# Kernel tuning notes

Hardware: AMD Instinct MI355X
Metric: run time of the kernel (lower is better)

## Reference

```python
import jax, jax.numpy as jnp
import numpy as np

B, L, D = 4, 512, 2880          # packed sequences, tokens per seq, hidden
N, K, H = 64, 8, 64             # query heads, kv heads, head dim
G = N // K                      # GQA group size
WINDOW = 128                    # sliding window (gpt-oss window layer)
SM_SCALE = 1.0 / H ** 0.5
THETA = 150000.0
INIT_CTX = 4096.0
SCALING = 32.0
NTK_ALPHA = 1.0
NTK_BETA = 32.0
NEG = -1e30


def _rope_tables(positions):
    # GPT-OSS YaRN NTK-by-parts rotary tables.
    d_half = H // 2
    freq = THETA ** (jnp.arange(0, H, 2, dtype=jnp.float32) / H)
    concentration = 0.1 * np.log(SCALING) + 1.0
    low = d_half * np.log(INIT_CTX / (NTK_BETA * 2 * np.pi)) / np.log(THETA)
    high = d_half * np.log(INIT_CTX / (NTK_ALPHA * 2 * np.pi)) / np.log(THETA)
    interp = 1.0 / (SCALING * freq)
    extrap = 1.0 / freq
    ramp = jnp.clip((jnp.arange(d_half, dtype=jnp.float32) - low) / (high - low), 0.0, 1.0)
    blend = 1.0 - ramp
    inv_freq = interp * (1.0 - blend) + extrap * blend
    ang = positions.astype(jnp.float32)[:, None] * inv_freq[None, :]  # [T, H/2]
    return jnp.cos(ang) * concentration, jnp.sin(ang) * concentration


def _apply_rope(x, cos, sin):
    # x: [T, heads, H]; half-split rotation as in gpt-oss.
    x1, x2 = x[..., : H // 2], x[..., H // 2:]
    c, s = cos[:, None, :], sin[:, None, :]
    return jnp.concatenate([x1 * c - x2 * s, x2 * c + x1 * s], axis=-1)


def setup_inputs() -> dict:
    key = jax.random.key(0)
    ks = jax.random.split(key, 10)
    T = B * L
    return {
        "x": jax.random.normal(ks[0], (T, D), jnp.float32),
        "wq": jax.random.normal(ks[1], (D, N, H), jnp.float32) * 0.02,
        "bq": jax.random.normal(ks[2], (N, H), jnp.float32) * 0.02,
        "wk": jax.random.normal(ks[3], (D, K, H), jnp.float32) * 0.02,
        "bk": jax.random.normal(ks[4], (K, H), jnp.float32) * 0.02,
        "wv": jax.random.normal(ks[5], (D, K, H), jnp.float32) * 0.02,
        "bv": jax.random.normal(ks[6], (K, H), jnp.float32) * 0.02,
        "wo": jax.random.normal(ks[7], (N, H, D), jnp.float32) * 0.02,
        "bo": jax.random.normal(ks[8], (D,), jnp.float32) * 0.02,
        "sinks": jax.random.normal(ks[9], (N,), jnp.float32),
        "positions": jnp.tile(jnp.arange(L, dtype=jnp.int32), B),  # per-seq positions
    }


def reference(x, wq, bq, wk, bk, wv, bv, wo, bo, sinks, positions):
    # fused QKV projections
    q = jnp.einsum('td,dnh->tnh', x, wq) + bq            # [T,N,H]
    k = jnp.einsum('td,dkh->tkh', x, wk) + bk            # [T,K,H]
    v = jnp.einsum('td,dkh->tkh', x, wv) + bv            # [T,K,H]
    cos, sin = _rope_tables(positions)
    q = _apply_rope(q, cos, sin)
    k = _apply_rope(k, cos, sin)
    # unpack ragged tokens into [B, L, ...] (equal-length packed sequences)
    qb = q.reshape(B, L, K, G, H)
    kb = k.reshape(B, L, K, H)
    vb = v.reshape(B, L, K, H)
    s = jnp.einsum('blkgh,bmkh->bkglm', qb, kb) * SM_SCALE  # [B,K,G,L,L]
    pos = jnp.arange(L)
    delta = pos[:, None] - pos[None, :]
    allowed = (delta >= 0) & (delta < WINDOW)               # causal + sliding window
    s = jnp.where(allowed, s, NEG)
    # attention sinks: extra per-head logit joining the softmax denominator only
    sink = sinks.reshape(K, G)[None, :, :, None]            # [1,K,G,1]
    m = jnp.maximum(jnp.max(s, axis=-1), sink)              # [B,K,G,L]
    p = jnp.exp(s - m[..., None])
    denom = jnp.exp(sink - m) + jnp.sum(p, axis=-1)         # [B,K,G,L]
    o = jnp.einsum('bkglm,bmkh->blkgh', p, vb)
    o = o / jnp.transpose(denom, (0, 3, 1, 2))[..., None]   # [B,L,K,G,H]
    attn = o.reshape(B * L, N, H)
    return jnp.einsum('tnh,nhd->td', attn, wo) + bo         # [T,D]
```

## Files before the change

### kernel.cpp

```cpp
#include <hip/hip_runtime.h>
#include <hip/hip_bf16.h>

#define TB 4
#define TL 512
#define TD 2880
#define TN 64
#define TKH 8
#define TH 64
#define TG 8
#define TWIN 128
#define TT (TB*TL)

typedef unsigned short u16;
typedef __attribute__((ext_vector_type(8))) short bf16x8;
typedef __attribute__((ext_vector_type(4))) float f32x4;

__device__ __forceinline__ u16 f2b(float f) {
  unsigned u = __float_as_uint(f);
  u += 0x7fffu + ((u >> 16) & 1u);
  return (u16)(u >> 16);
}
__device__ __forceinline__ float b2f(u16 u) {
  return __uint_as_float(((unsigned)u) << 16);
}

__device__ __forceinline__ void load_lds16(const u16* g, u16* l) {
  __builtin_amdgcn_global_load_lds(
      (const __attribute__((address_space(1))) unsigned int*)g,
      (__attribute__((address_space(3))) unsigned int*)l, 16, 0, 0);
}

template<int BN>
__global__ __launch_bounds__(256, 4) void gemm_sn(
    const u16* __restrict__ A, const u16* __restrict__ Bt,
    const float* __restrict__ bias, void* __restrict__ Cv,
    int Kd, int Nc, int ldc, int out_bf16, int nx)
{
  constexpr int NF = BN / 32;
  __shared__ u16 As[128*64];
  __shared__ u16 Bs[BN*64];

  const int tid  = threadIdx.x;
  const int lane = tid & 63;
  const int wave = tid >> 6;

  int id = blockIdx.x;
  const int cpx = gridDim.x >> 3;
  id = (id & 7)*cpx + (id >> 3);
  const int rgsz = nx << 3;
  const int rg   = id / rgsz;
  const int rem  = id - rg*rgsz;
  const int bm = (rg*8 + (rem & 7)) * 128;
  const int bn = (rem >> 3) * BN;

  const int wr = (wave >> 1) * 64;
  const int wc = (wave & 1) * (BN/2);

  f32x4 acc[4][NF];
#pragma unroll
  for (int i = 0; i < 4; ++i)
#pragma unroll
    for (int j = 0; j < NF; ++j) acc[i][j] = (f32x4){0.f,0.f,0.f,0.f};

  const int rr   = tid >> 3;
  const int sseg = (tid & 7) ^ (rr & 7);
  const u16* aS = A  + (size_t)(bm + rr)*Kd + sseg*8;
  const u16* bS = Bt + (size_t)(bn + rr)*Kd + sseg*8;

  const int fr = lane & 15, kq = lane >> 4;
  const int swz = lane & 7;

  const int NT = Kd >> 6;
  for (int t = 0; t < NT; ++t) {
    const int k0 = t << 6;
#pragma unroll
    for (int i = 0; i < 4; ++i)
      load_lds16(aS + (size_t)i*32*Kd + k0, &As[i*2048 + wave*512]);
#pragma unroll
    for (int i = 0; i < BN/32; ++i)
      load_lds16(bS + (size_t)i*32*Kd + k0, &Bs[i*2048 + wave*512]);
    __syncthreads();

#pragma unroll
    for (int s = 0; s < 2; ++s) {
      const int ch = ((s*4 + kq) ^ swz) * 16;
      bf16x8 af[4], bv[NF];
#pragma unroll
      for (int mi = 0; mi < 4; ++mi) {
        const int row = wr + mi*16 + fr;
        af[mi] = *(const bf16x8*)((const char*)&As[row*64] + ch);
      }
#pragma unroll
      for (int ni = 0; ni < NF; ++ni) {
        const int row = wc + ni*16 + fr;
        bv[ni] = *(const bf16x8*)((const char*)&Bs[row*64] + ch);
      }
#pragma unroll
      for (int mi = 0; mi < 4; ++mi)
#pragma unroll
        for (int ni = 0; ni < NF; ++ni)
          acc[mi][ni] = __builtin_amdgcn_mfma_f32_16x16x32_bf16(
              af[mi], bv[ni], acc[mi][ni], 0, 0, 0);
    }
    __syncthreads();
  }

  const int rbase = bm + wr + (lane >> 4)*4;
  const int cbase = bn + wc + (lane & 15);
#pragma unroll
  for (int mi = 0; mi < 4; ++mi) {
#pragma unroll
    for (int ni = 0; ni < NF; ++ni) {
      const int col = cbase + ni*16;
      const float bvl = (col < Nc) ? bias[col] : 0.f;
#pragma unroll
      for (int j = 0; j < 4; ++j) {
        const int row = rbase + mi*16 + j;
        const float val = acc[mi][ni][j] + bvl;
        if (out_bf16) {
          ((u16*)Cv)[(size_t)row*ldc + col] = f2b(val);
        } else if (col < Nc) {
          ((float*)Cv)[(size_t)row*ldc + col] = val;
        }
      }
    }
  }
}

__device__ __forceinline__ void tconv_into(
    float (*tile)[33], const float* __restrict__ in, u16* __restrict__ out,
    int R, int C, int bx, int by, int tid)
{
  const int c0 = bx*32, r0 = by*32;
  const int tx = tid & 31, ty = tid >> 5;
#pragma unroll
  for (int i = 0; i < 4; ++i)
    tile[ty + i*8][tx] = in[(size_t)(r0 + ty + i*8)*C + c0 + tx];
  __syncthreads();
#pragma unroll
  for (int i = 0; i < 4; ++i) {
    const int oc = ty + i*8;
    out[(size_t)(c0 + oc)*R + r0 + tx] = f2b(tile[tx][oc]);
  }
}

__global__ __launch_bounds__(256) void prep_kernel(
    const float* __restrict__ x,  const float* __restrict__ wq,
    const float* __restrict__ wk, const float* __restrict__ wv,
    const float* __restrict__ wo, const float* __restrict__ bq,
    const float* __restrict__ bk, const float* __restrict__ bv,
    u16* __restrict__ xb, u16* __restrict__ wqkvt, u16* __restrict__ wot,
    float* __restrict__ bqkv)
{
  __shared__ float tile[32][33];
  const int b = blockIdx.x;
  const int tid = threadIdx.x;

  if (b < 5760) {
    const int i = b*256 + tid;
    float4 f = ((const float4*)x)[i];
    ushort4 o;
    o.x = f2b(f.x); o.y = f2b(f.y); o.z = f2b(f.z); o.w = f2b(f.w);
    ((ushort4*)xb)[i] = o;
  } else if (b < 17280) {
    const int local = b - 5760;
    tconv_into(tile, wq, wqkvt, TD, 4096, local % 128, local / 128, tid);
  } else if (b < 18720) {
    const int local = b - 17280;
    tconv_into(tile, wk, wqkvt + (size_t)4096*TD, TD, 512,
               local % 16, local / 16, tid);
  } else if (b < 20160) {
    const int local = b - 18720;
    tconv_into(tile, wv, wqkvt + (size_t)4608*TD, TD, 512,
               local % 16, local / 16, tid);
  } else if (b < 31680) {
    const int local = b - 20160;
    tconv_into(tile, wo, wot, 4096, TD, local % 90, local / 90, tid);
  } else if (b < 31936) {
    const int i = (b - 31680)*256 + tid;
    ((ushort4*)(wot + (size_t)2880*4096))[i] = (ushort4){0,0,0,0};
  } else {
    const int i = (b - 31936)*256 + tid;
    if (i < 5120)
      bqkv[i] = (i < 4096) ? bq[i] : (i < 4608 ? bk[i-4096] : bv[i-4608]);
  }
}

__global__ __launch_bounds__(256) void rope_bf16_kernel(
    u16* __restrict__ qkv, const int* __restrict__ positions)
{
  const int total = TT*(TN+TKH)*32;
  int idx = blockIdx.x*256 + threadIdx.x;
  if (idx >= total) return;
  const int i    = idx & 31;
  const int rest = idx >> 5;
  const int head = rest % (TN+TKH);
  const int t    = rest / (TN+TKH);

  const float lnth = 11.918390573078392f;
  const float low  = 8.092779f;
  const float high = 17.398025f;
  const float conc = 1.3465735903f;

  const float fi = (float)i * 0.03125f;
  const float inv_theta_pow = __expf(-fi * lnth);
  const float interp = inv_theta_pow * (1.0f/32.0f);
  const float extrap = inv_theta_pow;
  float ramp = ((float)i - low) * (1.0f/(high - low));
  ramp = fminf(fmaxf(ramp, 0.0f), 1.0f);
  const float inv_freq = interp*ramp + extrap*(1.0f - ramp);

  const float ang = (float)positions[t] * inv_freq;
  const float mul = (head < TN) ? (conc * 0.125f) : conc;
  const float c = cosf(ang) * mul;
  const float s = sinf(ang) * mul;

  const int col = (head < TN) ? head*64 : 4096 + (head - TN)*64;
  u16* base = qkv + (size_t)t*5120 + col;
  const float x1 = b2f(base[i]);
  const float x2 = b2f(base[i + 32]);
  base[i]      = f2b(x1*c - x2*s);
  base[i + 32] = f2b(x2*c + x1*s);
}

__global__ __launch_bounds__(512) void attn3_kernel(
    const u16* __restrict__ qkv, u16* __restrict__ obuf,
    const float* __restrict__ sinks)
{
  __shared__ u16 Kl[192*64];
  __shared__ u16 Vt[64*192];
  __shared__ u16 Pl[8][2048];

  const int lt = blockIdx.x, kh = blockIdx.y, b = blockIdx.z;
  const int l0 = lt*64;
  const int mstart = (l0 > 127) ? (l0 - 127) : 0;
  const int mcnt = l0 + 64 - mstart;
  const int NC = (mcnt + 31) >> 5;
  const int base = l0 - mstart;

  const int tid = threadIdx.x;
  const int lane = tid & 63;
  const int g = tid >> 6;
  const int lL = lane & 15;
  const int q = lane >> 4;

  {
    const u16* kv0 = qkv + ((size_t)(b*TL + mstart)*5120 + 4096 + kh*64);
    for (int s = tid; s < 1536; s += 512) {
      const int m = s >> 3, hs = s & 7;
      uint4 kx = make_uint4(0,0,0,0), vx = make_uint4(0,0,0,0);
      if (m < mcnt) {
        const u16* gp = kv0 + (size_t)m*5120 + hs*8;
        kx = *(const uint4*)gp;
        vx = *(const uint4*)(gp + 512);
      }
      *(uint4*)((char*)&Kl[m*64] + ((hs*16) ^ ((m&7)<<4))) = kx;
      const unsigned vw[4] = {vx.x, vx.y, vx.z, vx.w};
#pragma unroll
      for (int i = 0; i < 8; ++i) {
        const int h = hs*8 + i;
        const u16 val = (u16)(vw[i>>1] >> ((i&1)*16));
        *(u16*)((char*)&Vt[h*192] + ((m*2) ^ (((h>>3)&7)<<4))) = val;
      }
    }
  }

  bf16x8 qb[4][2];
  {
    const u16* qbase = qkv + ((size_t)(b*TL + l0)*5120 + (kh*8 + g)*64);
#pragma unroll
    for (int l4 = 0; l4 < 4; ++l4)
#pragma unroll
      for (int kk = 0; kk < 2; ++kk)
        qb[l4][kk] = *(const bf16x8*)(qbase + (size_t)(l4*16 + lL)*5120 + kk*32 + q*8);
  }
  const float sink = sinks[kh*8 + g];
  __syncthreads();

  float Mrun[4] = {-1e30f,-1e30f,-1e30f,-1e30f};
  float Dden[4] = {0.f,0.f,0.f,0.f};
  f32x4 oacc[4][4];
#pragma unroll
  for (int i = 0; i < 4; ++i)
#pragma unroll
    for (int j = 0; j < 4; ++j) oacc[i][j] = (f32x4){0.f,0.f,0.f,0.f};

  u16* Pw = &Pl[g][0];

  for (int c = 0; c < NC; ++c) {
    bf16x8 ka[2][2];
#pragma unroll
    for (int m2 = 0; m2 < 2; ++m2) {
      const int row = c*32 + m2*16 + lL;
#pragma unroll
      for (int kk = 0; kk < 2; ++kk)
        ka[m2][kk] = *(const bf16x8*)((char*)&Kl[row*64] +
                       ((kk*64 + q*16) ^ ((row&7)<<4)));
    }
    bf16x8 vb[4];
#pragma unroll
    for (int hf = 0; hf < 4; ++hf) {
      const int h = hf*16 + lL;
      vb[hf] = *(const bf16x8*)((char*)&Vt[h*192] +
                 ((c*64 + q*16) ^ (((h>>3)&7)<<4)));
    }

#pragma unroll
    for (int l4 = 0; l4 < 4; ++l4) {
      const int lo = base + l4*16;
      if (c*32 > lo + 15 || c*32 + 31 < lo - 127) continue;

      const f32x4 z = (f32x4){0.f,0.f,0.f,0.f};
      f32x4 s0 = __builtin_amdgcn_mfma_f32_16x16x32_bf16(ka[0][0], qb[l4][0], z, 0,0,0);
      s0 = __builtin_amdgcn_mfma_f32_16x16x32_bf16(ka[0][1], qb[l4][1], s0, 0,0,0);
      f32x4 s1 = __builtin_amdgcn_mfma_f32_16x16x32_bf16(ka[1][0], qb[l4][0], z, 0,0,0);
      s1 = __builtin_amdgcn_mfma_f32_16x16x32_bf16(ka[1][1], qb[l4][1], s1, 0,0,0);

      float sv[2][4];
      bool  al[2][4];
      float cmax = -1e30f;
#pragma unroll
      for (int m2 = 0; m2 < 2; ++m2)
#pragma unroll
        for (int j = 0; j < 4; ++j) {
          const int delta = (lo + lL) - (c*32 + m2*16 + q*4 + j);
          const bool a = (delta >= 0) && (delta < TWIN);
          const float s = (m2 ? s1[j] : s0[j]);
          sv[m2][j] = s;
          al[m2][j] = a;
          if (a) cmax = fmaxf(cmax, s);
        }
      cmax = fmaxf(cmax, __shfl_xor(cmax, 16));
      cmax = fmaxf(cmax, __shfl_xor(cmax, 32));
      const float Mn = fmaxf(Mrun[l4], cmax);
      const float r = __expf(Mrun[l4] - Mn);
      Mrun[l4] = Mn;

      float ls = 0.f;
      u16 pb[2][4];
#pragma unroll
      for (int m2 = 0; m2 < 2; ++m2)
#pragma unroll
        for (int j = 0; j < 4; ++j) {
          const float p = al[m2][j] ? __expf(sv[m2][j] - Mn) : 0.f;
          ls += p;
          pb[m2][j] = f2b(p);
        }
      ls += __shfl_xor(ls, 16);
      ls += __shfl_xor(ls, 32);
      Dden[l4] = Dden[l4]*r + ls;

      const int l = l4*16 + lL;
#pragma unroll
      for (int m2 = 0; m2 < 2; ++m2) {
        uint2 w;
        w.x = (unsigned)pb[m2][0] | ((unsigned)pb[m2][1] << 16);
        w.y = (unsigned)pb[m2][2] | ((unsigned)pb[m2][3] << 16);
        *(uint2*)((char*)Pw + l*64 + ((m2*32 + q*8) ^ ((l&3)<<4))) = w;
      }

      float rb[4];
#pragma unroll
      for (int j = 0; j < 4; ++j) rb[j] = __shfl(r, q*4 + j);
#pragma unroll
      for (int hf = 0; hf < 4; ++hf)
#pragma unroll
        for (int j = 0; j < 4; ++j) oacc[l4][hf][j] *= rb[j];

      bf16x8 pa = *(const bf16x8*)((char*)Pw + l*64 + ((q*16) ^ ((l&3)<<4)));
#pragma unroll
      for (int hf = 0; hf < 4; ++hf)
        oacc[l4][hf] = __builtin_amdgcn_mfma_f32_16x16x32_bf16(
            pa, vb[hf], oacc[l4][hf], 0, 0, 0);
    }
  }

#pragma unroll
  for (int l4 = 0; l4 < 4; ++l4) {
    const float di = 1.0f / (Dden[l4] + __expf(sink - Mrun[l4]));
    float db[4];
#pragma unroll
    for (int j = 0; j < 4; ++j) db[j] = __shfl(di, q*4 + j);
#pragma unroll
    for (int hf = 0; hf < 4; ++hf)
#pragma unroll
      for (int j = 0; j < 4; ++j) {
        const int row = l0 + l4*16 + q*4 + j;
        obuf[(size_t)(b*TL + row)*4096 + (kh*8 + g)*64 + hf*16 + lL] =
            f2b(oacc[l4][hf][j] * db[j]);
      }
  }
}

extern "C" void kernel_launch(void* const* d_in, const int* in_sizes, int n_in,
                              void* d_out, int out_size, void* d_ws, size_t ws_size,
                              hipStream_t stream)
{
  const float* x     = (const float*)d_in[0];
  const float* wq    = (const float*)d_in[1];
  const float* bq    = (const float*)d_in[2];
  const float* wk    = (const float*)d_in[3];
  const float* bk    = (const float*)d_in[4];
  const float* wv    = (const float*)d_in[5];
  const float* bv    = (const float*)d_in[6];
  const float* wo    = (const float*)d_in[7];
  const float* bo    = (const float*)d_in[8];
  const float* sinks = (const float*)d_in[9];
  const int* positions = (const int*)d_in[10];
  float* out = (float*)d_out;

  u16* xb    = (u16*)d_ws;
  u16* wqkvt = xb + (size_t)TT*TD;
  u16* wot   = wqkvt + (size_t)5120*TD;
  u16* qkv   = wot + (size_t)2944*4096;
  u16* obuf  = qkv + (size_t)TT*5120;
  float* bqkv = (float*)(obuf + (size_t)TT*4096);

  prep_kernel<<<31956, 256, 0, stream>>>(
      x, wq, wk, wv, wo, bq, bk, bv, xb, wqkvt, wot, bqkv);

  gemm_sn<64><<<1280, 256, 0, stream>>>(
      xb, wqkvt, bqkv, qkv, TD, 5120, 5120, 1, 80);

  rope_bf16_kernel<<<(TT*(TN+TKH)*32 + 255)/256, 256, 0, stream>>>(qkv, positions);

  attn3_kernel<<<dim3(8, TKH, TB), 512, 0, stream>>>(qkv, obuf, sinks);

  gemm_sn<64><<<720, 256, 0, stream>>>(
      obuf, wot, bo, out, 4096, 2880, 2880, 0, 45);
}
```

Before: 205.0 us.

## Split-K output projection into bf16 partials with a separate reduction kernel

Replaces the output-projection GEMM (720 blocks) with a two-way split-K GEMM that writes bf16 partial sums into the now-unused qkv and xb buffers. A new reduction kernel then adds the two partials and the bias into the fp32 output. The aim is to double the number of blocks so the 256 CUs are better occupied. The cost is an extra kernel launch, more memory traffic, and bf16 rounding of the partials before they are summed. Launch bounds also rise from 4 to 6 blocks per CU for both GEMMs, which may push register usage down.

```diff
diff --git a/kernel.cpp b/kernel.cpp
--- a/kernel.cpp
+++ b/kernel.cpp
@@ -31,7 +31,7 @@
 }
 
 template<int BN>
-__global__ __launch_bounds__(256, 4) void gemm_sn(
+__global__ __launch_bounds__(256, 6) void gemm_sn(
     const u16* __restrict__ A, const u16* __restrict__ Bt,
     const float* __restrict__ bias, void* __restrict__ Cv,
     int Kd, int Nc, int ldc, int out_bf16, int nx)
@@ -125,6 +125,126 @@
       }
     }
   }
+}
+
+template<int BN>
+__global__ __launch_bounds__(256, 6) void gemm_skn(
+    const u16* __restrict__ A, const u16* __restrict__ Bt,
+    u16* __restrict__ P0, u16* __restrict__ P1,
+    int Kd, int ksplit, int Nc, int nx)
+{
+  constexpr int NF = BN / 32;
+  __shared__ u16 As[128*64];
+  __shared__ u16 Bs[BN*64];
+
+  const int tid  = threadIdx.x;
+  const int lane = tid & 63;
+  const int wave = tid >> 6;
+
+  int id = blockIdx.x;
+  const int cpx = gridDim.x >> 3;
+  id = (id & 7)*cpx + (id >> 3);
+  const int rgsz = nx << 3;
+  const int rg   = id / rgsz;
+  const int rem  = id - rg*rgsz;
+  const int bm = (rg*8 + (rem & 7)) * 128;
+  const int bn = (rem >> 3) * BN;
+
+  const int sp = blockIdx.y;
+  const int kstart = sp * ksplit;
+  const int NT = ksplit >> 6;
+
+  const int wr = (wave >> 1) * 64;
+  const int wc = (wave & 1) * (BN/2);
+
+  f32x4 acc[4][NF];
+#pragma unroll
+  for (int i = 0; i < 4; ++i)
+#pragma unroll
+    for (int j = 0; j < NF; ++j) acc[i][j] = (f32x4){0.f,0.f,0.f,0.f};
+
+  const int rr   = tid >> 3;
+  const int sseg = (tid & 7) ^ (rr & 7);
+  const u16* aS = A  + (size_t)(bm + rr)*Kd + kstart + sseg*8;
+  const u16* bS = Bt + (size_t)(bn + rr)*Kd + kstart + sseg*8;
+
+  const int fr = lane & 15, kq = lane >> 4;
+  const int swz = lane & 7;
+
+  for (int t = 0; t < NT; ++t) {
+    const int k0 = t << 6;
+#pragma unroll
+    for (int i = 0; i < 4; ++i)
+      load_lds16(aS + (size_t)i*32*Kd + k0, &As[i*2048 + wave*512]);
+#pragma unroll
+    for (int i = 0; i < BN/32; ++i)
+      load_lds16(bS + (size_t)i*32*Kd + k0, &Bs[i*2048 + wave*512]);
+    __syncthreads();
+
+#pragma unroll
+    for (int s = 0; s < 2; ++s) {
+      const int ch = ((s*4 + kq) ^ swz) * 16;
+      bf16x8 af[4], bv[NF];
+#pragma unroll
+      for (int mi = 0; mi < 4; ++mi) {
+        const int row = wr + mi*16 + fr;
+        af[mi] = *(const bf16x8*)((const char*)&As[row*64] + ch);
+      }
+#pragma unroll
+      for (int ni = 0; ni < NF; ++ni) {
+        const int row = wc + ni*16 + fr;
+        bv[ni] = *(const bf16x8*)((const char*)&Bs[row*64] + ch);
+      }
+#pragma unroll
+      for (int mi = 0; mi < 4; ++mi)
+#pragma unroll
+        for (int ni = 0; ni < NF; ++ni)
+          acc[mi][ni] = __builtin_amdgcn_mfma_f32_16x16x32_bf16(
+              af[mi], bv[ni], acc[mi][ni], 0, 0, 0);
+    }
+    __syncthreads();
+  }
+
+  u16* Pv = sp ? P1 : P0;
+  const int rbase = bm + wr + (lane >> 4)*4;
+  const int cbase = bn + wc + (lane & 15);
+#pragma unroll
+  for (int mi = 0; mi < 4; ++mi) {
+#pragma unroll
+    for (int ni = 0; ni < NF; ++ni) {
+      const int col = cbase + ni*16;
+      if (col < Nc) {
+#pragma unroll
+        for (int j = 0; j < 4; ++j) {
+          const int row = rbase + mi*16 + j;
+          Pv[(size_t)row*Nc + col] = f2b(acc[mi][ni][j]);
+        }
+      }
+    }
+  }
+}
+
+__global__ __launch_bounds__(256) void redout_kernel(
+    const u16* __restrict__ P0, const u16* __restrict__ P1,
+    const float* __restrict__ bo, float* __restrict__ out)
+{
+  const int i = blockIdx.x*256 + threadIdx.x;
+  const size_t e8 = (size_t)i * 8;
+  const int col0 = (int)(e8 % 2880);
+
+  float4 b0 = *(const float4*)&bo[col0];
+  float4 b1 = *(const float4*)&bo[col0 + 4];
+  float v[8] = {b0.x, b0.y, b0.z, b0.w, b1.x, b1.y, b1.z, b1.w};
+
+  uint4 a = *(const uint4*)(P0 + e8);
+  uint4 c = *(const uint4*)(P1 + e8);
+  const unsigned aw[4] = {a.x,a.y,a.z,a.w}, cw[4] = {c.x,c.y,c.z,c.w};
+#pragma unroll
+  for (int j = 0; j < 8; ++j)
+    v[j] += b2f((u16)(aw[j>>1] >> ((j&1)*16))) +
+            b2f((u16)(cw[j>>1] >> ((j&1)*16)));
+  *(float4*)&out[e8]     = make_float4(v[0],v[1],v[2],v[3]);
+  *(float4*)&out[e8 + 4] = make_float4(v[4],v[5],v[6],v[7]);
 }
 
 __device__ __forceinline__ void tconv_into(
@@ -416,6 +536,9 @@
   u16* obuf  = qkv + (size_t)TT*5120;
   float* bqkv = (float*)(obuf + (size_t)TT*4096);
 
+  u16* oP0 = qkv;
+  u16* oP1 = xb;
+
   prep_kernel<<<31956, 256, 0, stream>>>(
       x, wq, wk, wv, wo, bq, bk, bv, xb, wqkvt, wot, bqkv);
 
@@ -426,6 +549,8 @@
 
   attn3_kernel<<<dim3(8, TKH, TB), 512, 0, stream>>>(qkv, obuf, sinks);
 
-  gemm_sn<64><<<720, 256, 0, stream>>>(
-      obuf, wot, bo, out, 4096, 2880, 2880, 0, 45);
-}
+  gemm_skn<64><<<dim3(720, 2), 256, 0, stream>>>(
+      obuf, wot, oP0, oP1, 4096, 2048, 2880, 45);
+
+  redout_kernel<<<2880, 256, 0, stream>>>(oP0, oP1, bo, out);
+}
```

New measurement: 218.4 us. +6.5%, slower.

## Fuse RoPE into QKV GEMM epilogue and double-buffer GEMM K-loop

Applied to the files above, without the earlier changes.

Removes the standalone RoPE kernel and applies the rotary embedding in the QKV projection GEMM's epilogue. It remaps the wave column layout so each lane holds both halves (i and i+32) of a head dim, which also saves a full read/write pass over the qkv buffer. The GEMM now uses a double-buffered 32-wide K tile with async global-to-LDS prefetch, explicit vmcnt waits and raised MFMA priority, so loads overlap compute. Occupancy target goes from 4 to 6 blocks. The cost is more loop iterations with smaller tiles, plus per-element sin/cos in the epilogue.

```diff
diff --git a/kernel.cpp b/kernel.cpp
--- a/kernel.cpp
+++ b/kernel.cpp
@@ -30,15 +30,16 @@
       (__attribute__((address_space(3))) unsigned int*)l, 16, 0, 0);
 }
 
-template<int BN>
-__global__ __launch_bounds__(256, 4) void gemm_sn(
+template<int BN, int ROPE>
+__global__ __launch_bounds__(256, 6) void gemm_db(
     const u16* __restrict__ A, const u16* __restrict__ Bt,
     const float* __restrict__ bias, void* __restrict__ Cv,
+    const int* __restrict__ positions,
     int Kd, int Nc, int ldc, int out_bf16, int nx)
 {
   constexpr int NF = BN / 32;
-  __shared__ u16 As[128*64];
-  __shared__ u16 Bs[BN*64];
+  __shared__ u16 As[2][128*32];
+  __shared__ u16 Bs[2][BN*32];
 
   const int tid  = threadIdx.x;
   const int lane = tid & 63;
@@ -54,7 +55,8 @@
   const int bn = (rem >> 3) * BN;
 
   const int wr = (wave >> 1) * 64;
-  const int wc = (wave & 1) * (BN/2);
+  const int wc = ROPE ? (wave & 1) * 16 : (wave & 1) * (BN/2);
+  constexpr int NSTR = ROPE ? 32 : 16;
 
   f32x4 acc[4][NF];
 #pragma unroll
@@ -62,65 +64,119 @@
 #pragma unroll
     for (int j = 0; j < NF; ++j) acc[i][j] = (f32x4){0.f,0.f,0.f,0.f};
 
-  const int rr   = tid >> 3;
-  const int sseg = (tid & 7) ^ (rr & 7);
+  const int rr   = tid >> 2;
+  const int sseg = (tid & 3) ^ ((rr >> 1) & 3);
   const u16* aS = A  + (size_t)(bm + rr)*Kd + sseg*8;
   const u16* bS = Bt + (size_t)(bn + rr)*Kd + sseg*8;
 
+#define STG(dc, kt) do {                                         \
+    const int _k0 = (kt) << 5;                                   \
+    load_lds16(aS + _k0,                    &As[dc][wave*512]);  \
+    load_lds16(aS + (size_t)64*Kd + _k0,    &As[dc][2048 + wave*512]); \
+    load_lds16(bS + _k0,                    &Bs[dc][wave*512]);  \
+  } while (0)
+
   const int fr = lane & 15, kq = lane >> 4;
-  const int swz = lane & 7;
-
-  const int NT = Kd >> 6;
+  const int sx = (fr >> 1) & 3;
+
+  const int NT = Kd >> 5;
+  STG(0, 0);
+
   for (int t = 0; t < NT; ++t) {
-    const int k0 = t << 6;
-#pragma unroll
-    for (int i = 0; i < 4; ++i)
-      load_lds16(aS + (size_t)i*32*Kd + k0, &As[i*2048 + wave*512]);
-#pragma unroll
-    for (int i = 0; i < BN/32; ++i)
-      load_lds16(bS + (size_t)i*32*Kd + k0, &Bs[i*2048 + wave*512]);
-    __syncthreads();
-
-#pragma unroll
-    for (int s = 0; s < 2; ++s) {
-      const int ch = ((s*4 + kq) ^ swz) * 16;
-      bf16x8 af[4], bv[NF];
-#pragma unroll
-      for (int mi = 0; mi < 4; ++mi) {
-        const int row = wr + mi*16 + fr;
-        af[mi] = *(const bf16x8*)((const char*)&As[row*64] + ch);
-      }
-#pragma unroll
-      for (int ni = 0; ni < NF; ++ni) {
-        const int row = wc + ni*16 + fr;
-        bv[ni] = *(const bf16x8*)((const char*)&Bs[row*64] + ch);
-      }
-#pragma unroll
-      for (int mi = 0; mi < 4; ++mi)
-#pragma unroll
-        for (int ni = 0; ni < NF; ++ni)
-          acc[mi][ni] = __builtin_amdgcn_mfma_f32_16x16x32_bf16(
-              af[mi], bv[ni], acc[mi][ni], 0, 0, 0);
-    }
-    __syncthreads();
-  }
+    const int c = t & 1;
+    if (t + 1 < NT) {
+      STG(c ^ 1, t + 1);
+      asm volatile("s_waitcnt vmcnt(3)" ::: "memory");
+    } else {
+      asm volatile("s_waitcnt vmcnt(0)" ::: "memory");
+    }
+    __builtin_amdgcn_s_barrier();
+    __builtin_amdgcn_sched_barrier(0);
+
+    bf16x8 af[4], bv[NF];
+#pragma unroll
+    for (int mi = 0; mi < 4; ++mi) {
+      const int row = wr + mi*16 + fr;
+      af[mi] = *(const bf16x8*)((const char*)&As[c][row*32] + ((kq ^ sx) << 4));
+    }
+#pragma unroll
+    for (int ni = 0; ni < NF; ++ni) {
+      const int row = wc + ni*NSTR + fr;
+      bv[ni] = *(const bf16x8*)((const char*)&Bs[c][row*32] + ((kq ^ sx) << 4));
+    }
+    __builtin_amdgcn_s_setprio(1);
+#pragma unroll
+    for (int mi = 0; mi < 4; ++mi)
+#pragma unroll
+      for (int ni = 0; ni < NF; ++ni)
+        acc[mi][ni] = __builtin_amdgcn_mfma_f32_16x16x32_bf16(
+            af[mi], bv[ni], acc[mi][ni], 0, 0, 0);
+    __builtin_amdgcn_s_setprio(0);
+
+    __builtin_amdgcn_s_barrier();
+    __builtin_amdgcn_sched_barrier(0);
+  }
+#undef STG
 
   const int rbase = bm + wr + (lane >> 4)*4;
-  const int cbase = bn + wc + (lane & 15);
-#pragma unroll
-  for (int mi = 0; mi < 4; ++mi) {
-#pragma unroll
-    for (int ni = 0; ni < NF; ++ni) {
-      const int col = cbase + ni*16;
-      const float bvl = (col < Nc) ? bias[col] : 0.f;
+
+  if (ROPE) {
+    const int i = wc + (lane & 15);
+    const int col1 = bn + i, col2 = col1 + 32;
+    const int htype = (bn < 4096) ? 0 : (bn < 4608 ? 1 : 2);
+    const float b1 = bias[col1], b2 = bias[col2];
+
+    float invf = 0.f, mul = 0.f;
+    if (htype < 2) {
+      const float lnth = 11.918390573078392f;
+      const float low  = 8.092779f;
+      const float high = 17.398025f;
+      const float conc = 1.3465735903f;
+      const float fi = (float)i * 0.03125f;
+      const float itp = __expf(-fi * lnth);
+      float ramp = ((float)i - low) * (1.0f/(high - low));
+      ramp = fminf(fmaxf(ramp, 0.0f), 1.0f);
+      invf = itp*(1.0f/32.0f)*ramp + itp*(1.0f - ramp);
+      mul = (htype == 0) ? (conc * 0.125f) : conc;
+    }
+
+    u16* Cb = (u16*)Cv;
+#pragma unroll
+    for (int mi = 0; mi < 4; ++mi) {
 #pragma unroll
       for (int j = 0; j < 4; ++j) {
         const int row = rbase + mi*16 + j;
-        const float val = acc[mi][ni][j] + bvl;
-        if (out_bf16) {
-          ((u16*)Cv)[(size_t)row*ldc + col] = f2b(val);
-        } else if (col < Nc) {
-          ((float*)Cv)[(size_t)row*ldc + col] = val;
+        float x1 = acc[mi][0][j] + b1;
+        float x2 = acc[mi][1][j] + b2;
+        if (htype < 2) {
+          const float ang = (float)positions[row] * invf;
+          const float cc = cosf(ang) * mul;
+          const float ss = sinf(ang) * mul;
+          const float y1 = x1*cc - x2*ss;
+          const float y2 = x2*cc + x1*ss;
+          x1 = y1; x2 = y2;
+        }
+        Cb[(size_t)row*ldc + col1] = f2b(x1);
+        Cb[(size_t)row*ldc + col2] = f2b(x2);
+      }
+    }
+  } else {
+    const int cbase = bn + wc + (lane & 15);
+#pragma unroll
+    for (int mi = 0; mi < 4; ++mi) {
+#pragma unroll
+      for (int ni = 0; ni < NF; ++ni) {
+        const int col = cbase + ni*NSTR;
+        const float bvl = (col < Nc) ? bias[col] : 0.f;
+#pragma unroll
+        for (int j = 0; j < 4; ++j) {
+          const int row = rbase + mi*16 + j;
+          const float val = acc[mi][ni][j] + bvl;
+          if (out_bf16) {
+            ((u16*)Cv)[(size_t)row*ldc + col] = f2b(val);
+          } else if (col < Nc) {
+            ((float*)Cv)[(size_t)row*ldc + col] = val;
+          }
         }
       }
     }
@@ -186,43 +242,6 @@
   }
 }
 
-__global__ __launch_bounds__(256) void rope_bf16_kernel(
-    u16* __restrict__ qkv, const int* __restrict__ positions)
-{
-  const int total = TT*(TN+TKH)*32;
-  int idx = blockIdx.x*256 + threadIdx.x;
-  if (idx >= total) return;
-  const int i    = idx & 31;
-  const int rest = idx >> 5;
-  const int head = rest % (TN+TKH);
-  const int t    = rest / (TN+TKH);
-
-  const float lnth = 11.918390573078392f;
-  const float low  = 8.092779f;
-  const float high = 17.398025f;
-  const float conc = 1.3465735903f;
-
-  const float fi = (float)i * 0.03125f;
-  const float inv_theta_pow = __expf(-fi * lnth);
-  const float interp = inv_theta_pow * (1.0f/32.0f);
-  const float extrap = inv_theta_pow;
-  float ramp = ((float)i - low) * (1.0f/(high - low));
-  ramp = fminf(fmaxf(ramp, 0.0f), 1.0f);
-  const float inv_freq = interp*ramp + extrap*(1.0f - ramp);
-
-  const float ang = (float)positions[t] * inv_freq;
-  const float mul = (head < TN) ? (conc * 0.125f) : conc;
-  const float c = cosf(ang) * mul;
-  const float s = sinf(ang) * mul;
-
-  const int col = (head < TN) ? head*64 : 4096 + (head - TN)*64;
-  u16* base = qkv + (size_t)t*5120 + col;
-  const float x1 = b2f(base[i]);
-  const float x2 = b2f(base[i + 32]);
-  base[i]      = f2b(x1*c - x2*s);
-  base[i + 32] = f2b(x2*c + x1*s);
-}
-
 __global__ __launch_bounds__(512) void attn3_kernel(
     const u16* __restrict__ qkv, u16* __restrict__ obuf,
     const float* __restrict__ sinks)
@@ -419,13 +438,11 @@
   prep_kernel<<<31956, 256, 0, stream>>>(
       x, wq, wk, wv, wo, bq, bk, bv, xb, wqkvt, wot, bqkv);
 
-  gemm_sn<64><<<1280, 256, 0, stream>>>(
-      xb, wqkvt, bqkv, qkv, TD, 5120, 5120, 1, 80);
-
-  rope_bf16_kernel<<<(TT*(TN+TKH)*32 + 255)/256, 256, 0, stream>>>(qkv, positions);
+  gemm_db<64, 1><<<1280, 256, 0, stream>>>(
+      xb, wqkvt, bqkv, qkv, positions, TD, 5120, 5120, 1, 80);
 
   attn3_kernel<<<dim3(8, TKH, TB), 512, 0, stream>>>(qkv, obuf, sinks);
 
-  gemm_sn<64><<<720, 256, 0, stream>>>(
-      obuf, wot, bo, out, 4096, 2880, 2880, 0, 45);
-}
+  gemm_db<64, 0><<<720, 256, 0, stream>>>(
+      obuf, wot, bo, out, nullptr, 4096, 2880, 2880, 0, 45);
+}
```

Result: slower. 233.0 us (+13.6%).
